# Kernel optimization log

Measured on AMD Instinct MI355X. Metric: run time of the kernel, lower is better.

## Reference

```python
import jax, jax.numpy as jnp
import numpy as np

B, C, H, W = 4, 64, 64, 64

def setup_inputs() -> dict:
    key = jax.random.key(0)
    ks = jax.random.split(key, 7)
    s = 1.0 / np.sqrt(C)
    return {
        "x": jax.random.normal(ks[0], (B, C, H, W), dtype=jnp.float32),
        "Wq": jax.random.normal(ks[1], (C, C), dtype=jnp.float32) * s,
        "bq": jax.random.normal(ks[2], (C,), dtype=jnp.float32) * s,
        "Wk": jax.random.normal(ks[3], (C, C), dtype=jnp.float32) * s,
        "bk": jax.random.normal(ks[4], (C,), dtype=jnp.float32) * s,
        "Wv": jax.random.normal(ks[5], (C, C), dtype=jnp.float32) * s,
        "bv": jax.random.normal(ks[6], (C,), dtype=jnp.float32) * s,
    }

def reference(x, Wq, bq, Wk, bk, Wv, bv):
    b, c, h, w = x.shape
    n = h * w
    xf = x.reshape(b, c, n)                                   # (B,C,N)
    # 1x1 convs == per-pixel linear maps over channels
    q = jnp.einsum('oc,bcn->bon', Wq, xf) + bq[None, :, None]  # (B,C,N)
    k = jnp.einsum('oc,bcn->bon', Wk, xf) + bk[None, :, None]  # (B,C,N)
    v = jnp.einsum('oc,bcn->bon', Wv, xf) + bv[None, :, None]  # (B,C,N)
    # energy = Q^T K : (B,N,N); note: no 1/sqrt(C) scaling in the original
    energy = jnp.einsum('bcn,bcm->bnm', q, k)
    attention = jax.nn.softmax(energy, axis=-1)
    # out = V @ attention^T : out[:, :, i] = sum_j V[:, :, j] * attention[i, j]
    out = jnp.einsum('bcm,bnm->bcn', v, attention)
    return out.reshape(b, c, h, w)
```

## Files before the change

### kernel.cpp

```cpp
#include <hip/hip_runtime.h>
#include <math.h>

#define T_N 4096
#define T_C 64
#define T_B 4
#define NSLICE 4
#define TILES_PER_SLICE (64 / NSLICE)

typedef __attribute__((ext_vector_type(8))) _Float16 f16x8;
typedef __attribute__((ext_vector_type(4))) _Float16 f16x4;
typedef __attribute__((ext_vector_type(4))) float f32x4;

__device__ inline unsigned short f2h(float f) {
    union { _Float16 h; unsigned short s; } u; u.h = (_Float16)f; return u.s;
}
__device__ inline float h2f(unsigned short s) {
    union { unsigned short s; _Float16 h; } u; u.s = s; return (float)u.h;
}

__global__ __launch_bounds__(256) void qkv_kernel(
    const float* __restrict__ x,
    const float* __restrict__ Wq, const float* __restrict__ bq,
    const float* __restrict__ Wk, const float* __restrict__ bk,
    const float* __restrict__ Wv, const float* __restrict__ bv,
    unsigned short* __restrict__ qt_hi, unsigned short* __restrict__ qt_lo,
    unsigned short* __restrict__ kt, unsigned short* __restrict__ vb)
{
    __shared__ __align__(16) unsigned short xsh[32 * 72];
    __shared__ __align__(16) unsigned short xsl[32 * 72];
    __shared__ __align__(16) unsigned short wf[3][64 * 72];

    const int tid = threadIdx.x;
    const int n0  = blockIdx.x * 32;
    const int b   = blockIdx.y;
    const float* xb = x + (size_t)b * T_C * T_N;

    const float* Ws[3] = {Wq, Wk, Wv};
    #pragma unroll
    for (int p = 0; p < 3; ++p) {
        for (int i = tid; i < 1024; i += 256) {
            const int o = i >> 4, c4 = (i & 15) * 4;
            const float4 w4 = ((const float4*)Ws[p])[i];
            f16x4 wh;
            wh[0] = (_Float16)w4.x; wh[1] = (_Float16)w4.y;
            wh[2] = (_Float16)w4.z; wh[3] = (_Float16)w4.w;
            *(f16x4*)&wf[p][o * 72 + c4] = wh;
        }
    }
    for (int i = tid; i < 512; i += 256) {
        const int c = i >> 3, nj4 = (i & 7) * 4;
        const float4 xv = *(const float4*)&xb[c * T_N + n0 + nj4];
        const float xa[4] = {xv.x, xv.y, xv.z, xv.w};
        #pragma unroll
        for (int j = 0; j < 4; ++j) {
            const unsigned short h = f2h(xa[j]);
            xsh[(nj4 + j) * 72 + c] = h;
            xsl[(nj4 + j) * 72 + c] = f2h(xa[j] - h2f(h));
        }
    }
    __syncthreads();

    const int wv_  = tid >> 6;
    const int lane = tid & 63;
    const int quad = lane >> 4;
    const int col  = lane & 15;
    const int pst  = (wv_ & 1) * 16;
    const int oh   = (wv_ >> 1) * 2;
    const size_t bN = (size_t)b * T_N;

    f16x8 xh[2], xl[2];
    #pragma unroll
    for (int s = 0; s < 2; ++s) {
        xh[s] = *(const f16x8*)&xsh[(pst + col) * 72 + s * 32 + quad * 8];
        xl[s] = *(const f16x8*)&xsl[(pst + col) * 72 + s * 32 + quad * 8];
    }
    __syncthreads();

    const float* biases[3] = {bq, bk, bv};
    for (int p = 0; p < 3; ++p) {
        #pragma unroll
        for (int oo = 0; oo < 2; ++oo) {
            const int osub = oh + oo;
            f32x4 acc = (f32x4){0.f, 0.f, 0.f, 0.f};
            #pragma unroll
            for (int s = 0; s < 2; ++s) {
                const f16x8 wfr =
                    *(const f16x8*)&wf[p][(osub * 16 + col) * 72 + s * 32 + quad * 8];
                acc = __builtin_amdgcn_mfma_f32_16x16x32_f16(xh[s], wfr, acc, 0, 0, 0);
                acc = __builtin_amdgcn_mfma_f32_16x16x32_f16(xl[s], wfr, acc, 0, 0, 0);
            }
            const float bb = biases[p][osub * 16 + col];
            if (p == 0) {
                #pragma unroll
                for (int r = 0; r < 4; ++r) {
                    const float f = acc[r] + bb;
                    const unsigned short h = f2h(f);
                    const int a = (pst + quad * 4 + r) * 72 + osub * 16 + col;
                    xsh[a] = h;
                    xsl[a] = f2h(f - h2f(h));
                }
            } else if (p == 1) {
                #pragma unroll
                for (int r = 0; r < 4; ++r)
                    xsh[(pst + quad * 4 + r) * 72 + osub * 16 + col] = f2h(acc[r] + bb);
            } else {
                union { ushort4 v; unsigned short s[4]; } hv;
                #pragma unroll
                for (int r = 0; r < 4; ++r) hv.s[r] = f2h(acc[r] + bb);
                *(ushort4*)&xsh[(osub * 16 + col) * 36 + pst + quad * 4] = hv.v;
            }
        }
        __syncthreads();
        if (p == 0) {
            const int pix = tid >> 3, c8 = (tid & 7) * 8;
            *(f16x8*)&qt_hi[(bN + n0 + pix) * 64 + c8] = *(const f16x8*)&xsh[pix * 72 + c8];
            *(f16x8*)&qt_lo[(bN + n0 + pix) * 64 + c8] = *(const f16x8*)&xsl[pix * 72 + c8];
        } else if (p == 1) {
            const int pix = tid >> 3, c8 = (tid & 7) * 8;
            *(f16x8*)&kt[(bN + n0 + pix) * 64 + c8] = *(const f16x8*)&xsh[pix * 72 + c8];
        } else {
            const int o = tid >> 2, p8 = (tid & 3) * 8;
            *(f16x8*)&vb[((size_t)(b * 64 + o)) * T_N + n0 + p8] =
                *(const f16x8*)&xsh[o * 36 + p8];
        }
        if (p < 2) __syncthreads();
    }
}

__global__ __launch_bounds__(256, 4) void attn_kernel(
    const unsigned short* __restrict__ qt_hi, const unsigned short* __restrict__ qt_lo,
    const unsigned short* __restrict__ kt, const unsigned short* __restrict__ vb,
    unsigned short* __restrict__ o_part, float* __restrict__ mp, float* __restrict__ lp)
{
    __shared__ __align__(16) unsigned short ks[64 * 72];
    __shared__ __align__(16) unsigned short vs[64 * 72];

    const int tid   = threadIdx.x;
    const int n0    = blockIdx.x * 64;
    const int slice = blockIdx.y;
    const int b     = blockIdx.z;
    const int wv_   = tid >> 6;
    const int lane  = tid & 63;
    const int quad  = lane >> 4;
    const int col   = lane & 15;

    const size_t bN = (size_t)b * T_N;
    const int q_own = n0 + wv_ * 16 + col;

    f16x8 qh[2], ql[2];
    #pragma unroll
    for (int s = 0; s < 2; ++s) {
        const size_t qoff = (bN + q_own) * 64 + s * 32 + quad * 8;
        qh[s] = *(const f16x8*)&qt_hi[qoff];
        ql[s] = *(const f16x8*)&qt_lo[qoff];
    }

    f32x4 O[4];
    #pragma unroll
    for (int t = 0; t < 4; ++t) O[t] = (f32x4){0.f, 0.f, 0.f, 0.f};
    float m_st = -INFINITY, l_st = 0.f;

    for (int it = 0; it < TILES_PER_SLICE; ++it) {
        const int m0 = (slice * TILES_PER_SLICE + it) * 64;
        __syncthreads();
        for (int i = tid; i < 1024; i += 256) {
            if (i < 512) {
                const int row = i >> 3, cc = i & 7;
                *(float4*)&ks[row * 72 + cc * 8] =
                    *(const float4*)&kt[(bN + m0 + row) * 64 + cc * 8];
            } else {
                const int j = i - 512, row = j >> 3, cc = j & 7;
                *(float4*)&vs[row * 72 + cc * 8] =
                    *(const float4*)&vb[((size_t)(b * 64 + row)) * T_N + m0 + cc * 8];
            }
        }
        __syncthreads();

        f32x4 acc[4];
        #pragma unroll
        for (int t = 0; t < 4; ++t) acc[t] = (f32x4){0.f, 0.f, 0.f, 0.f};
        #pragma unroll
        for (int s = 0; s < 2; ++s) {
            #pragma unroll
            for (int t = 0; t < 4; ++t) {
                const f16x8 kf =
                    *(const f16x8*)&ks[(t * 16 + col) * 72 + s * 32 + quad * 8];
                acc[t] = __builtin_amdgcn_mfma_f32_16x16x32_f16(kf, qh[s], acc[t], 0, 0, 0);
                acc[t] = __builtin_amdgcn_mfma_f32_16x16x32_f16(kf, ql[s], acc[t], 0, 0, 0);
            }
        }

        float mx = -INFINITY;
        #pragma unroll
        for (int t = 0; t < 4; ++t)
            #pragma unroll
            for (int r = 0; r < 4; ++r) mx = fmaxf(mx, acc[t][r]);
        mx = fmaxf(mx, __shfl_xor(mx, 16));
        mx = fmaxf(mx, __shfl_xor(mx, 32));
        const float mnew = fmaxf(m_st, mx);
        const float alpha = __expf(m_st - mnew);
        float sum = 0.f;
        f16x4 pf[4];
        #pragma unroll
        for (int t = 0; t < 4; ++t) {
            #pragma unroll
            for (int r = 0; r < 4; ++r) {
                const float pv = __expf(acc[t][r] - mnew);
                sum += pv;
                pf[t][r] = (_Float16)pv;
            }
        }
        sum += __shfl_xor(sum, 16);
        sum += __shfl_xor(sum, 32);
        l_st = alpha * l_st + sum;
        m_st = mnew;

        #pragma unroll
        for (int tc = 0; tc < 4; ++tc) {
            O[tc] *= alpha;
            #pragma unroll
            for (int t = 0; t < 4; ++t) {
                const f16x4 vf =
                    *(const f16x4*)&vs[(tc * 16 + col) * 72 + t * 16 + quad * 4];
                O[tc] = __builtin_amdgcn_mfma_f32_16x16x16f16(vf, pf[t], O[tc], 0, 0, 0);
            }
        }
    }

    #pragma unroll
    for (int tc = 0; tc < 4; ++tc) {
        #pragma unroll
        for (int r = 0; r < 4; ++r) {
            o_part[((size_t)((slice * T_B + b) * 64 + tc * 16 + quad * 4 + r)) * T_N +
                   q_own] = f2h(O[tc][r]);
        }
    }
    if (quad == 0) {
        const size_t off = (size_t)(slice * T_B + b) * T_N + q_own;
        mp[off] = m_st;
        lp[off] = l_st;
    }
}

__global__ __launch_bounds__(256) void combine_kernel(
    const unsigned short* __restrict__ o_part,
    const float* __restrict__ mp, const float* __restrict__ lp,
    float* __restrict__ out)
{
    __shared__ float wn[NSLICE][32];

    const int tid = threadIdx.x;
    const int n0  = blockIdx.x * 32;
    const int b   = blockIdx.y;

    if (tid < 32) {
        float m_s[NSLICE], l_s[NSLICE];
        #pragma unroll
        for (int s = 0; s < NSLICE; ++s) {
            const size_t off = (size_t)(s * T_B + b) * T_N + n0 + tid;
            m_s[s] = mp[off];
            l_s[s] = lp[off];
        }
        float M = m_s[0];
        #pragma unroll
        for (int s = 1; s < NSLICE; ++s) M = fmaxf(M, m_s[s]);
        float w_s[NSLICE], L = 0.f;
        #pragma unroll
        for (int s = 0; s < NSLICE; ++s) {
            w_s[s] = __expf(m_s[s] - M);
            L += l_s[s] * w_s[s];
        }
        const float inv = 1.f / L;
        #pragma unroll
        for (int s = 0; s < NSLICE; ++s) wn[s][tid] = w_s[s] * inv;
    }
    __syncthreads();

    for (int t = tid; t < 512; t += 256) {
        const int c = t >> 3, g = t & 7;
        float4 acc = make_float4(0.f, 0.f, 0.f, 0.f);
        #pragma unroll
        for (int s = 0; s < NSLICE; ++s) {
            const ushort4 o4 = *(const ushort4*)
                &o_part[((size_t)((s * T_B + b) * 64 + c)) * T_N + n0 + g * 4];
            acc.x = fmaf(h2f(o4.x), wn[s][g * 4 + 0], acc.x);
            acc.y = fmaf(h2f(o4.y), wn[s][g * 4 + 1], acc.y);
            acc.z = fmaf(h2f(o4.z), wn[s][g * 4 + 2], acc.z);
            acc.w = fmaf(h2f(o4.w), wn[s][g * 4 + 3], acc.w);
        }
        *(float4*)&out[((size_t)(b * 64 + c)) * T_N + n0 + g * 4] = acc;
    }
}

extern "C" void kernel_launch(void* const* d_in, const int* in_sizes, int n_in,
                              void* d_out, int out_size, void* d_ws, size_t ws_size,
                              hipStream_t stream) {
    const float* x  = (const float*)d_in[0];
    const float* Wq = (const float*)d_in[1];
    const float* bq = (const float*)d_in[2];
    const float* Wk = (const float*)d_in[3];
    const float* bk = (const float*)d_in[4];
    const float* Wv = (const float*)d_in[5];
    const float* bv = (const float*)d_in[6];
    float* outp = (float*)d_out;

    const size_t elems = (size_t)T_B * T_N * T_C;
    unsigned short* qt_hi  = (unsigned short*)d_ws;
    unsigned short* qt_lo  = qt_hi + elems;
    unsigned short* ktp    = qt_lo + elems;
    unsigned short* vbuf   = ktp + elems;
    unsigned short* o_part = vbuf + elems;
    float* mp = (float*)(o_part + (size_t)NSLICE * elems);
    float* lp = mp + (size_t)NSLICE * T_B * T_N;

    qkv_kernel<<<dim3(T_N / 32, T_B), 256, 0, stream>>>(
        x, Wq, bq, Wk, bk, Wv, bv, qt_hi, qt_lo, ktp, vbuf);
    attn_kernel<<<dim3(T_N / 64, NSLICE, T_B), 256, 0, stream>>>(
        qt_hi, qt_lo, ktp, vbuf, o_part, mp, lp);
    combine_kernel<<<dim3(T_N / 32, T_B), 256, 0, stream>>>(
        o_part, mp, lp, outp);
}
```

Baseline: 129.7 us.

## Drop Q hi/lo split and prefetch next K/V tile into registers

Q is now stored as a single fp16 value instead of a hi/lo fp16 pair, which halves the QK^T MFMA count and removes one Q workspace buffer and its reads and writes. The attention loop also loads the next K/V tile from global memory into registers while the current tile is being computed, so load latency overlaps with the MFMAs. The price is lower precision in the un-scaled energy logits, which may hurt accuracy against the reference, plus extra register pressure.

```diff
diff --git a/kernel.cpp b/kernel.cpp
--- a/kernel.cpp
+++ b/kernel.cpp
@@ -23,8 +23,8 @@
     const float* __restrict__ Wq, const float* __restrict__ bq,
     const float* __restrict__ Wk, const float* __restrict__ bk,
     const float* __restrict__ Wv, const float* __restrict__ bv,
-    unsigned short* __restrict__ qt_hi, unsigned short* __restrict__ qt_lo,
-    unsigned short* __restrict__ kt, unsigned short* __restrict__ vb)
+    unsigned short* __restrict__ qt, unsigned short* __restrict__ kt,
+    unsigned short* __restrict__ vb)
 {
     __shared__ __align__(16) unsigned short xsh[32 * 72];
     __shared__ __align__(16) unsigned short xsl[32 * 72];
@@ -90,16 +90,7 @@
                 acc = __builtin_amdgcn_mfma_f32_16x16x32_f16(xl[s], wfr, acc, 0, 0, 0);
             }
             const float bb = biases[p][osub * 16 + col];
-            if (p == 0) {
-                #pragma unroll
-                for (int r = 0; r < 4; ++r) {
-                    const float f = acc[r] + bb;
-                    const unsigned short h = f2h(f);
-                    const int a = (pst + quad * 4 + r) * 72 + osub * 16 + col;
-                    xsh[a] = h;
-                    xsl[a] = f2h(f - h2f(h));
-                }
-            } else if (p == 1) {
+            if (p < 2) {
                 #pragma unroll
                 for (int r = 0; r < 4; ++r)
                     xsh[(pst + quad * 4 + r) * 72 + osub * 16 + col] = f2h(acc[r] + bb);
@@ -111,24 +102,21 @@
             }
         }
         __syncthreads();
-        if (p == 0) {
+        if (p < 2) {
             const int pix = tid >> 3, c8 = (tid & 7) * 8;
-            *(f16x8*)&qt_hi[(bN + n0 + pix) * 64 + c8] = *(const f16x8*)&xsh[pix * 72 + c8];
-            *(f16x8*)&qt_lo[(bN + n0 + pix) * 64 + c8] = *(const f16x8*)&xsl[pix * 72 + c8];
-        } else if (p == 1) {
-            const int pix = tid >> 3, c8 = (tid & 7) * 8;
-            *(f16x8*)&kt[(bN + n0 + pix) * 64 + c8] = *(const f16x8*)&xsh[pix * 72 + c8];
+            unsigned short* dst = (p == 0) ? qt : kt;
+            *(f16x8*)&dst[(bN + n0 + pix) * 64 + c8] = *(const f16x8*)&xsh[pix * 72 + c8];
+            __syncthreads();
         } else {
             const int o = tid >> 2, p8 = (tid & 3) * 8;
             *(f16x8*)&vb[((size_t)(b * 64 + o)) * T_N + n0 + p8] =
                 *(const f16x8*)&xsh[o * 36 + p8];
         }
-        if (p < 2) __syncthreads();
     }
 }
 
 __global__ __launch_bounds__(256, 4) void attn_kernel(
-    const unsigned short* __restrict__ qt_hi, const unsigned short* __restrict__ qt_lo,
+    const unsigned short* __restrict__ qt,
     const unsigned short* __restrict__ kt, const unsigned short* __restrict__ vb,
     unsigned short* __restrict__ o_part, float* __restrict__ mp, float* __restrict__ lp)
 {
@@ -147,12 +135,20 @@
     const size_t bN = (size_t)b * T_N;
     const int q_own = n0 + wv_ * 16 + col;
 
-    f16x8 qh[2], ql[2];
-    #pragma unroll
-    for (int s = 0; s < 2; ++s) {
-        const size_t qoff = (bN + q_own) * 64 + s * 32 + quad * 8;
-        qh[s] = *(const f16x8*)&qt_hi[qoff];
-        ql[s] = *(const f16x8*)&qt_lo[qoff];
+    f16x8 qh[2];
+    #pragma unroll
+    for (int s = 0; s < 2; ++s)
+        qh[s] = *(const f16x8*)&qt[(bN + q_own) * 64 + s * 32 + quad * 8];
+
+    const int row = tid >> 3, cc = tid & 7;
+
+    float4 pre[4];
+    {
+        const int m0 = slice * TILES_PER_SLICE * 64;
+        pre[0] = *(const float4*)&kt[(bN + m0 + row) * 64 + cc * 8];
+        pre[1] = *(const float4*)&kt[(bN + m0 + 32 + row) * 64 + cc * 8];
+        pre[2] = *(const float4*)&vb[((size_t)(b * 64 + row)) * T_N + m0 + cc * 8];
+        pre[3] = *(const float4*)&vb[((size_t)(b * 64 + 32 + row)) * T_N + m0 + cc * 8];
     }
 
     f32x4 O[4];
@@ -161,20 +157,20 @@
     float m_st = -INFINITY, l_st = 0.f;
 
     for (int it = 0; it < TILES_PER_SLICE; ++it) {
-        const int m0 = (slice * TILES_PER_SLICE + it) * 64;
         __syncthreads();
-        for (int i = tid; i < 1024; i += 256) {
-            if (i < 512) {
-                const int row = i >> 3, cc = i & 7;
-                *(float4*)&ks[row * 72 + cc * 8] =
-                    *(const float4*)&kt[(bN + m0 + row) * 64 + cc * 8];
-            } else {
-                const int j = i - 512, row = j >> 3, cc = j & 7;
-                *(float4*)&vs[row * 72 + cc * 8] =
-                    *(const float4*)&vb[((size_t)(b * 64 + row)) * T_N + m0 + cc * 8];
-            }
-        }
+        *(float4*)&ks[row * 72 + cc * 8]        = pre[0];
+        *(float4*)&ks[(32 + row) * 72 + cc * 8] = pre[1];
+        *(float4*)&vs[row * 72 + cc * 8]        = pre[2];
+        *(float4*)&vs[(32 + row) * 72 + cc * 8] = pre[3];
         __syncthreads();
+
+        if (it + 1 < TILES_PER_SLICE) {
+            const int m0n = (slice * TILES_PER_SLICE + it + 1) * 64;
+            pre[0] = *(const float4*)&kt[(bN + m0n + row) * 64 + cc * 8];
+            pre[1] = *(const float4*)&kt[(bN + m0n + 32 + row) * 64 + cc * 8];
+            pre[2] = *(const float4*)&vb[((size_t)(b * 64 + row)) * T_N + m0n + cc * 8];
+            pre[3] = *(const float4*)&vb[((size_t)(b * 64 + 32 + row)) * T_N + m0n + cc * 8];
+        }
 
         f32x4 acc[4];
         #pragma unroll
@@ -186,7 +182,6 @@
                 const f16x8 kf =
                     *(const f16x8*)&ks[(t * 16 + col) * 72 + s * 32 + quad * 8];
                 acc[t] = __builtin_amdgcn_mfma_f32_16x16x32_f16(kf, qh[s], acc[t], 0, 0, 0);
-                acc[t] = __builtin_amdgcn_mfma_f32_16x16x32_f16(kf, ql[s], acc[t], 0, 0, 0);
             }
         }
 
@@ -305,18 +300,17 @@
     float* outp = (float*)d_out;
 
     const size_t elems = (size_t)T_B * T_N * T_C;
-    unsigned short* qt_hi  = (unsigned short*)d_ws;
-    unsigned short* qt_lo  = qt_hi + elems;
-    unsigned short* ktp    = qt_lo + elems;
+    unsigned short* qtp    = (unsigned short*)d_ws;
+    unsigned short* ktp    = qtp + elems;
     unsigned short* vbuf   = ktp + elems;
     unsigned short* o_part = vbuf + elems;
     float* mp = (float*)(o_part + (size_t)NSLICE * elems);
     float* lp = mp + (size_t)NSLICE * T_B * T_N;
 
     qkv_kernel<<<dim3(T_N / 32, T_B), 256, 0, stream>>>(
-        x, Wq, bq, Wk, bk, Wv, bv, qt_hi, qt_lo, ktp, vbuf);
+        x, Wq, bq, Wk, bk, Wv, bv, qtp, ktp, vbuf);
     attn_kernel<<<dim3(T_N / 64, NSLICE, T_B), 256, 0, stream>>>(
-        qt_hi, qt_lo, ktp, vbuf, o_part, mp, lp);
+        qtp, ktp, vbuf, o_part, mp, lp);
     combine_kernel<<<dim3(T_N / 32, T_B), 256, 0, stream>>>(
         o_part, mp, lp, outp);
 }
```

Result: slower. 151.7 us (+16.9%).
